# Kernel tuning notes

Hardware: AMD Instinct MI355X
Metric: run time of the kernel (lower is better)

## Reference

```python
import jax, jax.numpy as jnp
import numpy as np

L = 4          # GAT_LAYERS
HEADS = 4      # N_HEADS
H = 64         # transformer hidden dim
DH = H // HEADS
FIN = 32       # NODE_EMBED_SIZE
A = 15         # gats.num_actions (readout size)
OBS = 1500     # flattened obs dim
HS = 512       # hidden_size (policy FC)
NOUT = 15      # num_outputs
VH = 128       # VALUE_HIDDENS
B = 128        # batch of graphs
N = 1000       # nodes per map graph
TOT = B * N
DEG = 4
E = TOT * DEG


def _lin(key, fan_in, shape):
    return jax.random.normal(key, shape, jnp.float32) * (1.0 / np.sqrt(fan_in))


def setup_inputs() -> dict:
    key = jax.random.key(0)
    ks = jax.random.split(key, 30)
    node_feats = jax.random.normal(ks[0], (TOT, FIN), jnp.float32)
    obs = jax.random.normal(ks[1], (B, OBS), jnp.float32)
    # batched-graph edges: endpoints stay within each graph (DGL batch semantics)
    off = (jnp.arange(B) * N)[:, None]
    edge_src = (jax.random.randint(ks[2], (B, N * DEG), 0, N) + off).reshape(-1).astype(jnp.int32)
    edge_dst = (jax.random.randint(ks[3], (B, N * DEG), 0, N) + off).reshape(-1).astype(jnp.int32)
    agent_nodes = (jax.random.randint(ks[4], (B,), 0, N) + jnp.arange(B) * N).astype(jnp.int32)
    p = {
        'W_in': _lin(ks[5], FIN, (FIN, H)),
        'Wq': _lin(ks[6], H, (L, H, H)), 'Wk': _lin(ks[7], H, (L, H, H)),
        'Wv': _lin(ks[8], H, (L, H, H)), 'Wo': _lin(ks[9], H, (L, H, H)),
        'ln1_g': jnp.ones((L, H), jnp.float32), 'ln1_b': jnp.zeros((L, H), jnp.float32),
        'W1': _lin(ks[10], H, (L, H, 2 * H)), 'b1': jnp.zeros((L, 2 * H), jnp.float32),
        'W2': _lin(ks[11], 2 * H, (L, 2 * H, H)), 'b2': jnp.zeros((L, H), jnp.float32),
        'ln2_g': jnp.ones((L, H), jnp.float32), 'ln2_b': jnp.zeros((L, H), jnp.float32),
        'Wr': _lin(ks[12], H, (H, A)), 'br': jnp.zeros((A,), jnp.float32),
        'Wp1': _lin(ks[13], A + OBS, (A + OBS, HS)), 'bp1': jnp.zeros((HS,), jnp.float32),
        'Wp2': _lin(ks[14], HS, (HS, HS)), 'bp2': jnp.zeros((HS,), jnp.float32),
        'Wlog': _lin(ks[15], HS, (HS, NOUT)), 'blog': jnp.zeros((NOUT,), jnp.float32),
        'Wv1': _lin(ks[16], OBS, (OBS, VH)), 'bv1': jnp.zeros((VH,), jnp.float32),
        'Wv2': _lin(ks[17], VH, (VH, VH)), 'bv2': jnp.zeros((VH,), jnp.float32),
        'Wvo': _lin(ks[18], VH, (VH, 1)), 'bvo': jnp.zeros((1,), jnp.float32),
    }
    return dict(node_feats=node_feats, obs=obs, edge_src=edge_src, edge_dst=edge_dst,
                agent_nodes=agent_nodes, **p)


def _layernorm(x, g, b):
    m = x.mean(-1, keepdims=True)
    v = ((x - m) ** 2).mean(-1, keepdims=True)
    return (x - m) * jax.lax.rsqrt(v + 1e-5) * g + b


def reference(node_feats, obs, edge_src, edge_dst, agent_nodes, W_in, Wq, Wk, Wv, Wo,
              ln1_g, ln1_b, W1, b1, W2, b2, ln2_g, ln2_b, Wr, br,
              Wp1, bp1, Wp2, bp2, Wlog, blog, Wv1, bv1, Wv2, bv2, Wvo, bvo):
    n = node_feats.shape[0]
    x = node_feats @ W_in                                   # [n, H]
    inv_sqrt_dh = np.float32(1.0 / np.sqrt(DH))
    for l in range(L):
        q = (x @ Wq[l]).reshape(n, HEADS, DH)
        k = (x @ Wk[l]).reshape(n, HEADS, DH)
        v = (x @ Wv[l]).reshape(n, HEADS, DH)
        # per-edge attention scores, softmax over incoming edges of each dst node
        s = jnp.sum(q[edge_dst] * k[edge_src], axis=-1) * inv_sqrt_dh   # [E, HEADS]
        m = jax.ops.segment_max(s, edge_dst, num_segments=n)            # [n, HEADS]
        w = jnp.exp(s - m[edge_dst])
        denom = jax.ops.segment_sum(w, edge_dst, num_segments=n)        # [n, HEADS]
        agg = jax.ops.segment_sum(w[:, :, None] * v[edge_src], edge_dst, num_segments=n)
        attn = (agg / (denom[:, :, None] + 1e-9)).reshape(n, H) @ Wo[l]
        x = _layernorm(x + attn, ln1_g[l], ln1_b[l])
        h = jax.nn.relu(x @ W1[l] + b1[l]) @ W2[l] + b2[l]
        x = _layernorm(x + h, ln2_g[l], ln2_b[l])
    gat_out = x[agent_nodes] @ Wr + br                      # [B, A] per-agent action features
    feat = jnp.tanh(jnp.concatenate([gat_out, obs], axis=1) @ Wp1 + bp1)
    feat = jnp.tanh(feat @ Wp2 + bp2)
    logits = feat @ Wlog + blog                             # [B, NOUT]
    vh = jnp.tanh(obs @ Wv1 + bv1)
    vh = jnp.tanh(vh @ Wv2 + bv2)
    value = (vh @ Wvo + bvo)[:, 0]                          # [B]
    return logits, value
```

## Files before the change

### kernel.cpp

```cpp
#include <hip/hip_runtime.h>
#include <hip/hip_bf16.h>
#include <cstdint>
#include <cstddef>

#define DEV static __device__ __forceinline__

constexpr int GRAPHS = 128;
constexpr int NPG    = 1000;
constexpr int EPG    = 4000;
constexpr int TOTN   = GRAPHS * NPG;
constexpr int TOTE   = GRAPHS * EPG;
constexpr int HD     = 64;
constexpr int OBSD   = 1500;
constexpr int AD     = 15;

typedef __attribute__((ext_vector_type(8))) short bf16x8;
typedef __attribute__((ext_vector_type(4))) float f32x4;

DEV unsigned short f2b(float f){
  unsigned u = __float_as_uint(f);
  return (unsigned short)((u + 0x7fffu + ((u >> 16) & 1u)) >> 16);
}
DEV float b2f(unsigned short s){ return __uint_as_float((unsigned)s << 16); }

DEV void fma4(float4& a, float s, const float4 w){
  a.x = fmaf(s, w.x, a.x); a.y = fmaf(s, w.y, a.y);
  a.z = fmaf(s, w.z, a.z); a.w = fmaf(s, w.w, a.w);
}

DEV ushort4 pack4(float4 v){
  ushort4 r; r.x=f2b(v.x); r.y=f2b(v.y); r.z=f2b(v.z); r.w=f2b(v.w); return r;
}

__global__ __launch_bounds__(256) void k_wprep(const float* __restrict__ Wq,
    const float* __restrict__ Wk, const float* __restrict__ Wv,
    const float* __restrict__ Wo, const float* __restrict__ W1,
    const float* __restrict__ W2, unsigned short* __restrict__ wpack){
  int e = blockIdx.x*256 + threadIdx.x;
  int l = e >> 15;
  int r = e & 32767;
  float val;
  if (r < 12288){
    int c = r >> 6, k = r & 63;
    val = (c < 64)  ? Wq[l*4096 + k*64 + c]
        : (c < 128) ? Wk[l*4096 + k*64 + (c-64)]
                    : Wv[l*4096 + k*64 + (c-128)];
  } else if (r < 16384){
    int i = r - 12288; int c = i >> 6, k = i & 63;
    val = Wo[l*4096 + k*64 + c];
  } else if (r < 24576){
    int i = r - 16384; int c = i >> 6, k = i & 63;
    val = W1[l*8192 + k*128 + c];
  } else {
    int i = r - 24576; int c = i >> 7, k = i & 127;
    val = W2[l*8192 + k*64 + c];
  }
  wpack[e] = f2b(val);
}

__global__ __launch_bounds__(256) void k_zero(int* __restrict__ cnt){
  cnt[blockIdx.x*256 + threadIdx.x] = 0;
}

__global__ __launch_bounds__(256) void k_hist(const int* __restrict__ edst,
                                              int* __restrict__ cnt){
  int e = blockIdx.x*256 + threadIdx.x;
  atomicAdd(&cnt[edst[e]], 1);
}

__global__ __launch_bounds__(1024) void k_scan(const int* __restrict__ cnt,
    int* __restrict__ rstart, int* __restrict__ cursor){
  __shared__ int s[1024];
  const int g = blockIdx.x, tid = threadIdx.x;
  int v = (tid < NPG) ? cnt[g*NPG + tid] : 0;
  s[tid] = v;
  __syncthreads();
  #pragma unroll
  for (int off=1; off<1024; off<<=1){
    int t = (tid >= off) ? s[tid-off] : 0;
    __syncthreads();
    s[tid] += t;
    __syncthreads();
  }
  if (tid < NPG){
    int r = g*EPG + (s[tid] - v);
    rstart[g*NPG+tid] = r;
    cursor[g*NPG+tid] = r;
  }
}

__global__ __launch_bounds__(256) void k_scatter(const int* __restrict__ esrc,
    const int* __restrict__ edst, int* __restrict__ cursor,
    int* __restrict__ esorted){
  int e = blockIdx.x*256 + threadIdx.x;
  int pos = atomicAdd(&cursor[edst[e]], 1);
  esorted[pos] = esrc[e];
}

__global__ __launch_bounds__(256) void k_in(const float* __restrict__ nf,
                                            const float* __restrict__ Win,
                                            unsigned short* __restrict__ xb){
  __shared__ float  s_nf[256*36];
  __shared__ float4 s_w[512];
  const int tid = threadIdx.x;
  const int node0 = blockIdx.x * 256;
  const float4* W4 = (const float4*)Win;
  s_w[tid] = W4[tid]; s_w[tid+256] = W4[tid+256];
  const float4* nf4 = (const float4*)nf;
  float4* snf4 = (float4*)s_nf;
  #pragma unroll
  for (int r=0;r<8;r++){
    int i = tid + 256*r; int n = i>>3, k4 = i&7;
    snf4[n*9 + k4] = nf4[(size_t)(node0+n)*8 + k4];
  }
  __syncthreads();
  const int ng = tid>>2, cg = tid&3;
  float4 acc[4][4];
  #pragma unroll
  for (int i=0;i<4;i++){ acc[i][0]=make_float4(0,0,0,0); acc[i][1]=make_float4(0,0,0,0);
                         acc[i][2]=make_float4(0,0,0,0); acc[i][3]=make_float4(0,0,0,0); }
  #pragma unroll 4
  for (int k=0;k<32;k++){
    float nv[4];
    #pragma unroll
    for (int i=0;i<4;i++) nv[i] = s_nf[(ng + 64*i)*36 + k];
    float4 w[4];
    #pragma unroll
    for (int j=0;j<4;j++) w[j] = s_w[k*16 + cg*4 + j];
    #pragma unroll
    for (int i=0;i<4;i++){
      #pragma unroll
      for (int j=0;j<4;j++) fma4(acc[i][j], nv[i], w[j]);
    }
  }
  ushort4* xb4 = (ushort4*)xb;
  #pragma unroll
  for (int i=0;i<4;i++){
    size_t nidx = (size_t)(node0 + ng + 64*i) * 16;
    #pragma unroll
    for (int j=0;j<4;j++) xb4[nidx + cg*4 + j] = pack4(acc[i][j]);
  }
}

__global__ __launch_bounds__(256) void k_qkv_m(const unsigned short* __restrict__ xb,
    const unsigned short* __restrict__ wqkvT,
    unsigned short* __restrict__ qkv){
  __shared__ short s_w[192*72];
  __shared__ short s_st[4][16*200];
  const int tid = threadIdx.x;
  const int node0 = blockIdx.x * 256;
  {
    const unsigned* src = (const unsigned*)wqkvT;
    unsigned* dst = (unsigned*)s_w;
    #pragma unroll
    for (int r=0;r<24;r++){
      int j = tid + 256*r;
      int c = j >> 5, kk = j & 31;
      dst[c*36 + kk] = src[j];
    }
  }
  __syncthreads();
  const int lane = tid & 63, wave = tid >> 6;
  const int m = lane & 15, quad = lane >> 4;
  const int rowbase = node0 + wave*64;
  bf16x8 af[4][2];
  #pragma unroll
  for (int rt=0;rt<4;rt++){
    const unsigned short* xp = xb + (size_t)(rowbase + rt*16 + m)*64 + quad*8;
    af[rt][0] = *(const bf16x8*)xp;
    af[rt][1] = *(const bf16x8*)(xp + 32);
  }
  short* st = s_st[wave];
  #pragma unroll
  for (int rt=0;rt<4;rt++){
    #pragma unroll
    for (int ct=0;ct<12;ct++){
      bf16x8 b0 = *(const bf16x8*)&s_w[(ct*16+m)*72 + quad*8];
      bf16x8 b1 = *(const bf16x8*)&s_w[(ct*16+m)*72 + 32 + quad*8];
      f32x4 acc = {0.f,0.f,0.f,0.f};
      acc = __builtin_amdgcn_mfma_f32_16x16x32_bf16(af[rt][0], b0, acc, 0,0,0);
      acc = __builtin_amdgcn_mfma_f32_16x16x32_bf16(af[rt][1], b1, acc, 0,0,0);
      #pragma unroll
      for (int i=0;i<4;i++)
        st[(quad*4+i)*200 + ct*16 + m] = (short)f2b(acc[i]);
    }
    #pragma unroll
    for (int j=0;j<6;j++){
      int flat = (j*64 + lane)*8;
      int r = flat / 192, c = flat % 192;
      bf16x8 v = *(const bf16x8*)&st[r*200 + c];
      *(bf16x8*)(qkv + (size_t)(rowbase + rt*16 + r)*192 + c) = v;
    }
  }
}

__global__ __launch_bounds__(256) void k_edge2(const unsigned short* __restrict__ qkv,
    const int* __restrict__ rstart, const int* __restrict__ cnt,
    const int* __restrict__ esorted, unsigned short* __restrict__ attn_in){
  const int tid = threadIdx.x;
  const int wb = (blockIdx.x & 7)*1000 + (blockIdx.x >> 3);
  const int lane = tid & 63;
  const int sub  = lane >> 4;
  const int dg   = lane & 15;
  const int wave = tid >> 6;
  const int node = wb*16 + wave*4 + sub;
  const ushort4* row = (const ushort4*)(qkv + (size_t)node*192);
  ushort4 qu = row[dg];
  float q0 = b2f(qu.x), q1 = b2f(qu.y), q2 = b2f(qu.z), q3 = b2f(qu.w);
  const int rs = rstart[node];
  const int n  = cnt[node];
  float a0=0.f, a1=0.f, a2=0.f, a3=0.f, den=0.f;
  for (int i=0;i<n;i++){
    int src = esorted[rs + i];
    ushort4 ku = *(const ushort4*)(qkv + (size_t)src*192 + 64 + dg*4);
    ushort4 vu = *(const ushort4*)(qkv + (size_t)src*192 + 128 + dg*4);
    float p = q0*b2f(ku.x) + q1*b2f(ku.y) + q2*b2f(ku.z) + q3*b2f(ku.w);
    p += __shfl_xor(p, 1);
    p += __shfl_xor(p, 2);
    float w = __expf(p * 0.25f);
    den += w;
    a0 = fmaf(w, b2f(vu.x), a0);
    a1 = fmaf(w, b2f(vu.y), a1);
    a2 = fmaf(w, b2f(vu.z), a2);
    a3 = fmaf(w, b2f(vu.w), a3);
  }
  float inv = 1.0f/(den + 1e-9f);
  ushort4 o;
  o.x = f2b(a0*inv); o.y = f2b(a1*inv); o.z = f2b(a2*inv); o.w = f2b(a3*inv);
  ((ushort4*)attn_in)[(size_t)node*16 + dg] = o;
}

__global__ __launch_bounds__(256) void k_attn_m(const unsigned short* __restrict__ attn_in,
    const unsigned short* __restrict__ woT, const float* __restrict__ lg,
    const float* __restrict__ lb, unsigned short* __restrict__ xb){
  __shared__ short s_w[64*72];
  __shared__ short s_st[4][16*72];
  const int tid = threadIdx.x;
  const int node0 = blockIdx.x*256;
  {
    const unsigned* src = (const unsigned*)woT;
    unsigned* dst = (unsigned*)s_w;
    #pragma unroll
    for (int r=0;r<8;r++){
      int j = tid + 256*r;
      int c = j >> 5, kk = j & 31;
      dst[c*36 + kk] = src[j];
    }
  }
  __syncthreads();
  const int lane = tid&63, wave = tid>>6;
  const int m = lane&15, quad = lane>>4;
  const int rowbase = node0 + wave*64;
  bf16x8 bf[4][2];
  #pragma unroll
  for (int ct=0;ct<4;ct++){
    bf[ct][0] = *(const bf16x8*)&s_w[(ct*16+m)*72 + quad*8];
    bf[ct][1] = *(const bf16x8*)&s_w[(ct*16+m)*72 + 32 + quad*8];
  }
  float g[4], bb[4];
  #pragma unroll
  for (int ct=0;ct<4;ct++){ g[ct]=lg[ct*16+m]; bb[ct]=lb[ct*16+m]; }
  short* st = s_st[wave];
  #pragma unroll
  for (int rt=0;rt<4;rt++){
    const unsigned short* ap = attn_in + (size_t)(rowbase + rt*16 + m)*64 + quad*8;
    bf16x8 a0 = *(const bf16x8*)ap;
    bf16x8 a1 = *(const bf16x8*)(ap + 32);
    f32x4 acc[4];
    #pragma unroll
    for (int ct=0;ct<4;ct++){
      f32x4 z = {0.f,0.f,0.f,0.f};
      z = __builtin_amdgcn_mfma_f32_16x16x32_bf16(a0, bf[ct][0], z, 0,0,0);
      z = __builtin_amdgcn_mfma_f32_16x16x32_bf16(a1, bf[ct][1], z, 0,0,0);
      acc[ct] = z;
    }
    #pragma unroll
    for (int i=0;i<4;i++){
      size_t row = (size_t)(rowbase + rt*16 + quad*4 + i)*64;
      float v0 = acc[0][i] + b2f(xb[row + m]);
      float v1 = acc[1][i] + b2f(xb[row + 16 + m]);
      float v2 = acc[2][i] + b2f(xb[row + 32 + m]);
      float v3 = acc[3][i] + b2f(xb[row + 48 + m]);
      float sm = v0+v1+v2+v3;
      float sq = v0*v0+v1*v1+v2*v2+v3*v3;
      #pragma unroll
      for (int mk=1; mk<16; mk<<=1){ sm += __shfl_xor(sm, mk); sq += __shfl_xor(sq, mk); }
      float mean = sm*0.015625f;
      float var  = sq*0.015625f - mean*mean;
      float rs   = rsqrtf(var + 1e-5f);
      int rl = quad*4 + i;
      st[rl*72 + m]      = (short)f2b((v0-mean)*rs*g[0]+bb[0]);
      st[rl*72 + 16 + m] = (short)f2b((v1-mean)*rs*g[1]+bb[1]);
      st[rl*72 + 32 + m] = (short)f2b((v2-mean)*rs*g[2]+bb[2]);
      st[rl*72 + 48 + m] = (short)f2b((v3-mean)*rs*g[3]+bb[3]);
    }
    #pragma unroll
    for (int j=0;j<2;j++){
      int flat = (j*64 + lane)*8;
      int r = flat >> 6, c = flat & 63;
      bf16x8 v = *(const bf16x8*)&st[r*72 + c];
      *(bf16x8*)(xb + (size_t)(rowbase + rt*16 + r)*64 + c) = v;
    }
  }
}

__global__ __launch_bounds__(256) void k_ffn1_m(const unsigned short* __restrict__ xb,
    const unsigned short* __restrict__ w1T, const float* __restrict__ b1_l,
    unsigned short* __restrict__ h){
  __shared__ short s_w[128*72];
  __shared__ short s_st[4][16*136];
  const int tid = threadIdx.x;
  const int node0 = blockIdx.x*256;
  {
    const unsigned* src = (const unsigned*)w1T;
    unsigned* dst = (unsigned*)s_w;
    #pragma unroll
    for (int r=0;r<16;r++){
      int j = tid + 256*r;
      int c = j >> 5, kk = j & 31;
      dst[c*36 + kk] = src[j];
    }
  }
  __syncthreads();
  const int lane = tid&63, wave = tid>>6;
  const int m = lane&15, quad = lane>>4;
  const int rowbase = node0 + wave*64;
  bf16x8 af[4][2];
  #pragma unroll
  for (int rt=0;rt<4;rt++){
    const unsigned short* xp = xb + (size_t)(rowbase + rt*16 + m)*64 + quad*8;
    af[rt][0] = *(const bf16x8*)xp;
    af[rt][1] = *(const bf16x8*)(xp + 32);
  }
  short* st = s_st[wave];
  #pragma unroll
  for (int rt=0;rt<4;rt++){
    #pragma unroll
    for (int ct=0;ct<8;ct++){
      bf16x8 b0 = *(const bf16x8*)&s_w[(ct*16+m)*72 + quad*8];
      bf16x8 b1 = *(const bf16x8*)&s_w[(ct*16+m)*72 + 32 + quad*8];
      float bias = b1_l[ct*16+m];
      f32x4 acc = {0.f,0.f,0.f,0.f};
      acc = __builtin_amdgcn_mfma_f32_16x16x32_bf16(af[rt][0], b0, acc, 0,0,0);
      acc = __builtin_amdgcn_mfma_f32_16x16x32_bf16(af[rt][1], b1, acc, 0,0,0);
      #pragma unroll
      for (int i=0;i<4;i++)
        st[(quad*4+i)*136 + ct*16 + m] = (short)f2b(fmaxf(acc[i]+bias, 0.f));
    }
    #pragma unroll
    for (int j=0;j<4;j++){
      int flat = (j*64 + lane)*8;
      int r = flat >> 7, c = flat & 127;
      bf16x8 v = *(const bf16x8*)&st[r*136 + c];
      *(bf16x8*)(h + (size_t)(rowbase + rt*16 + r)*128 + c) = v;
    }
  }
}

__global__ __launch_bounds__(256) void k_ffn2_m(const unsigned short* __restrict__ h,
    const unsigned short* __restrict__ w2T, const float* __restrict__ b2_l,
    const float* __restrict__ lg, const float* __restrict__ lb,
    unsigned short* __restrict__ xb){
  __shared__ short s_w[64*136];
  __shared__ short s_st[4][16*72];
  const int tid = threadIdx.x;
  const int node0 = blockIdx.x*256;
  {
    const unsigned* src = (const unsigned*)w2T;
    unsigned* dst = (unsigned*)s_w;
    #pragma unroll
    for (int r=0;r<16;r++){
      int j = tid + 256*r;
      int c = j >> 6, kk = j & 63;
      dst[c*68 + kk] = src[j];
    }
  }
  __syncthreads();
  const int lane = tid&63, wave = tid>>6;
  const int m = lane&15, quad = lane>>4;
  const int rowbase = node0 + wave*64;
  bf16x8 bf[4][4];
  #pragma unroll
  for (int ct=0;ct<4;ct++){
    #pragma unroll
    for (int kc=0;kc<4;kc++)
      bf[ct][kc] = *(const bf16x8*)&s_w[(ct*16+m)*136 + kc*32 + quad*8];
  }
  float g[4], bb[4], b2v[4];
  #pragma unroll
  for (int ct=0;ct<4;ct++){ g[ct]=lg[ct*16+m]; bb[ct]=lb[ct*16+m]; b2v[ct]=b2_l[ct*16+m]; }
  short* st = s_st[wave];
  #pragma unroll
  for (int rt=0;rt<4;rt++){
    const unsigned short* ap = h + (size_t)(rowbase + rt*16 + m)*128 + quad*8;
    bf16x8 a0 = *(const bf16x8*)ap;
    bf16x8 a1 = *(const bf16x8*)(ap + 32);
    bf16x8 a2 = *(const bf16x8*)(ap + 64);
    bf16x8 a3 = *(const bf16x8*)(ap + 96);
    f32x4 acc[4];
    #pragma unroll
    for (int ct=0;ct<4;ct++){
      f32x4 z = {0.f,0.f,0.f,0.f};
      z = __builtin_amdgcn_mfma_f32_16x16x32_bf16(a0, bf[ct][0], z, 0,0,0);
      z = __builtin_amdgcn_mfma_f32_16x16x32_bf16(a1, bf[ct][1], z, 0,0,0);
      z = __builtin_amdgcn_mfma_f32_16x16x32_bf16(a2, bf[ct][2], z, 0,0,0);
      z = __builtin_amdgcn_mfma_f32_16x16x32_bf16(a3, bf[ct][3], z, 0,0,0);
      acc[ct] = z;
    }
    #pragma unroll
    for (int i=0;i<4;i++){
      size_t row = (size_t)(rowbase + rt*16 + quad*4 + i)*64;
      float v0 = acc[0][i] + b2v[0] + b2f(xb[row + m]);
      float v1 = acc[1][i] + b2v[1] + b2f(xb[row + 16 + m]);
      float v2 = acc[2][i] + b2v[2] + b2f(xb[row + 32 + m]);
      float v3 = acc[3][i] + b2v[3] + b2f(xb[row + 48 + m]);
      float sm = v0+v1+v2+v3;
      float sq = v0*v0+v1*v1+v2*v2+v3*v3;
      #pragma unroll
      for (int mk=1; mk<16; mk<<=1){ sm += __shfl_xor(sm, mk); sq += __shfl_xor(sq, mk); }
      float mean = sm*0.015625f;
      float var  = sq*0.015625f - mean*mean;
      float rs   = rsqrtf(var + 1e-5f);
      int rl = quad*4 + i;
      st[rl*72 + m]      = (short)f2b((v0-mean)*rs*g[0]+bb[0]);
      st[rl*72 + 16 + m] = (short)f2b((v1-mean)*rs*g[1]+bb[1]);
      st[rl*72 + 32 + m] = (short)f2b((v2-mean)*rs*g[2]+bb[2]);
      st[rl*72 + 48 + m] = (short)f2b((v3-mean)*rs*g[3]+bb[3]);
    }
    #pragma unroll
    for (int j=0;j<2;j++){
      int flat = (j*64 + lane)*8;
      int r = flat >> 6, c = flat & 63;
      bf16x8 v = *(const bf16x8*)&st[r*72 + c];
      *(bf16x8*)(xb + (size_t)(rowbase + rt*16 + r)*64 + c) = v;
    }
  }
}

__global__ __launch_bounds__(256) void k_feat(const unsigned short* __restrict__ xb,
    const float* __restrict__ obs, const int* __restrict__ agents,
    const float* __restrict__ Wr, const float* __restrict__ br,
    float* __restrict__ feat){
  __shared__ float s_xa[64];
  const int b = blockIdx.x, tid = threadIdx.x;
  if (tid < 64) s_xa[tid] = b2f(xb[(size_t)agents[b]*HD + tid]);
  __syncthreads();
  if (tid < AD){
    float a = br[tid];
    #pragma unroll 8
    for (int k=0;k<HD;k++) a = fmaf(s_xa[k], Wr[k*AD + tid], a);
    feat[(size_t)b*1536 + tid] = a;
  }
  for (int i=tid;i<OBSD;i+=256) feat[(size_t)b*1536 + AD + i] = obs[(size_t)b*OBSD + i];
  if (tid < 21) feat[(size_t)b*1536 + 1515 + tid] = 0.f;
}

template<int ROWS, int COLS, int CH, int KS, int N>
__global__ __launch_bounds__(ROWS*COLS) void k_gemm_part(
    const float* __restrict__ A, int lda, int K,
    const float* __restrict__ W, float* __restrict__ part){
  constexpr int BT = ROWS*COLS;
  __shared__ float s_a[ROWS*CH];
  const int tid = threadIdx.x;
  const int ct = blockIdx.x, rg = blockIdx.y, ks = blockIdx.z;
  const int chunk = (K + KS - 1) / KS;
  const int k0 = ks * chunk;
  const int len = min(K - k0, chunk);
  const int row0 = rg * ROWS;
  #pragma unroll
  for (int rr=0; rr<ROWS; rr++)
    for (int i=tid; i<len; i+=BT)
      s_a[rr*CH + i] = A[(size_t)(row0+rr)*lda + k0 + i];
  __syncthreads();
  const int r = tid / COLS, c = tid % COLS;
  const float* wp = W + (size_t)k0*N + ct*COLS + c;
  const float* ap = s_a + r*CH;
  float acc = 0.f;
  #pragma unroll 8
  for (int k=0;k<len;k++) acc = fmaf(ap[k], wp[(size_t)k*N], acc);
  part[((size_t)ks*128 + row0 + r)*N + ct*COLS + c] = acc;
}

template<int KS, int N, bool TANH>
__global__ __launch_bounds__(256) void k_reduce(const float* __restrict__ part,
    const float* __restrict__ bias, float* __restrict__ out, int MN){
  const int idx = blockIdx.x*256 + threadIdx.x;
  if (idx >= MN) return;
  float s = bias[idx & (N-1)];
  #pragma unroll
  for (int ks=0;ks<KS;ks++) s += part[(size_t)ks*MN + idx];
  out[idx] = TANH ? tanhf(s) : s;
}

__global__ __launch_bounds__(256) void k_logits(const float* __restrict__ f2,
    const float* __restrict__ Wlog, const float* __restrict__ blog,
    float* __restrict__ out){
  __shared__ float s_f[512];
  __shared__ float s_p[16*AD];
  const int b = blockIdx.x, tid = threadIdx.x;
  s_f[tid]     = f2[(size_t)b*512 + tid];
  s_f[tid+256] = f2[(size_t)b*512 + 256 + tid];
  __syncthreads();
  if (tid < 240){
    int c = tid % AD, kc = tid / AD;
    float a = 0.f;
    #pragma unroll 8
    for (int j=0;j<32;j++){ int k = kc*32 + j; a = fmaf(s_f[k], Wlog[k*AD + c], a); }
    s_p[tid] = a;
  }
  __syncthreads();
  if (tid < AD){
    float a = blog[tid];
    #pragma unroll
    for (int kc=0;kc<16;kc++) a += s_p[kc*AD + tid];
    out[(size_t)b*AD + tid] = a;
  }
}

__global__ __launch_bounds__(128) void k_vfin(const float* __restrict__ vh,
    const float* __restrict__ Wv2, const float* __restrict__ bv2,
    const float* __restrict__ Wvo, const float* __restrict__ bvo,
    float* __restrict__ out){
  __shared__ float s_v[128];
  __shared__ float s_r[128];
  const int b = blockIdx.x, tid = threadIdx.x;
  s_v[tid] = vh[(size_t)b*128 + tid];
  __syncthreads();
  float a = bv2[tid];
  #pragma unroll 8
  for (int k=0;k<128;k++) a = fmaf(s_v[k], Wv2[k*128 + tid], a);
  s_r[tid] = tanhf(a) * Wvo[tid];
  __syncthreads();
  if (tid < 64){
    float v = s_r[tid] + s_r[tid+64];
    #pragma unroll
    for (int m=32;m>=1;m>>=1) v += __shfl_xor(v, m);
    if (tid==0) out[GRAPHS*AD + b] = v + bvo[0];
  }
}

extern "C" void kernel_launch(void* const* d_in, const int* in_sizes, int n_in,
                              void* d_out, int out_size, void* d_ws, size_t ws_size,
                              hipStream_t stream) {
  (void)in_sizes; (void)n_in; (void)out_size; (void)ws_size;
  const float* nf     = (const float*)d_in[0];
  const float* obs    = (const float*)d_in[1];
  const int*   esrc   = (const int*)d_in[2];
  const int*   edst   = (const int*)d_in[3];
  const int*   agents = (const int*)d_in[4];
  const float* Win    = (const float*)d_in[5];
  const float* Wq     = (const float*)d_in[6];
  const float* Wk     = (const float*)d_in[7];
  const float* Wv     = (const float*)d_in[8];
  const float* Wo     = (const float*)d_in[9];
  const float* ln1g   = (const float*)d_in[10];
  const float* ln1b   = (const float*)d_in[11];
  const float* W1     = (const float*)d_in[12];
  const float* b1     = (const float*)d_in[13];
  const float* W2     = (const float*)d_in[14];
  const float* b2     = (const float*)d_in[15];
  const float* ln2g   = (const float*)d_in[16];
  const float* ln2b   = (const float*)d_in[17];
  const float* Wr     = (const float*)d_in[18];
  const float* br     = (const float*)d_in[19];
  const float* Wp1    = (const float*)d_in[20];
  const float* bp1    = (const float*)d_in[21];
  const float* Wp2    = (const float*)d_in[22];
  const float* bp2    = (const float*)d_in[23];
  const float* Wlog   = (const float*)d_in[24];
  const float* blog   = (const float*)d_in[25];
  const float* Wv1    = (const float*)d_in[26];
  const float* bv1    = (const float*)d_in[27];
  const float* Wv2    = (const float*)d_in[28];
  const float* bv2    = (const float*)d_in[29];
  const float* Wvo    = (const float*)d_in[30];
  const float* bvo    = (const float*)d_in[31];
  float* out = (float*)d_out;

  unsigned short* xb      = (unsigned short*)d_ws;
  unsigned short* qkv     = xb + (size_t)TOTN*HD;
  unsigned short* hbuf    = qkv;
  unsigned short* attn_in = qkv + (size_t)TOTN*192;
  unsigned short* wpack   = attn_in + (size_t)TOTN*HD;
  int* cnt     = (int*)(wpack + 131072);
  int* rstart  = cnt + TOTN;
  int* cursor  = rstart + TOTN;
  int* esorted = cursor + TOTN;
  float* feat = (float*)(esorted + TOTE);
  float* f1   = feat + 128*1536;
  float* f2   = f1 + 128*512;
  float* vh   = f2 + 128*512;
  float* part = vh + 128*128;

  k_wprep  <<<512, 256, 0, stream>>>(Wq, Wk, Wv, Wo, W1, W2, wpack);
  k_zero   <<<TOTN/256, 256, 0, stream>>>(cnt);
  k_hist   <<<TOTE/256, 256, 0, stream>>>(edst, cnt);
  k_scan   <<<GRAPHS, 1024, 0, stream>>>(cnt, rstart, cursor);
  k_scatter<<<TOTE/256, 256, 0, stream>>>(esrc, edst, cursor, esorted);

  k_in<<<TOTN/256, 256, 0, stream>>>(nf, Win, xb);
  for (int l=0; l<4; l++){
    const unsigned short* wl = wpack + l*32768;
    k_qkv_m <<<TOTN/256, 256, 0, stream>>>(xb, wl, qkv);
    k_edge2 <<<TOTN/16, 256, 0, stream>>>(qkv, rstart, cnt, esorted, attn_in);
    k_attn_m<<<TOTN/256, 256, 0, stream>>>(attn_in, wl + 12288,
                                           ln1g + l*64, ln1b + l*64, xb);
    k_ffn1_m<<<TOTN/256, 256, 0, stream>>>(xb, wl + 16384, b1 + l*128, hbuf);
    k_ffn2_m<<<TOTN/256, 256, 0, stream>>>(hbuf, wl + 24576, b2 + l*64,
                                           ln2g + l*64, ln2b + l*64, xb);
  }
  k_feat<<<GRAPHS, 256, 0, stream>>>(xb, obs, agents, Wr, br, feat);
  k_gemm_part<2,256,384,4,512><<<dim3(2,64,4), 512, 0, stream>>>(feat, 1536, 1515, Wp1, part);
  k_reduce<4,512,true><<<256, 256, 0, stream>>>(part, bp1, f1, 128*512);
  k_gemm_part<2,256,256,2,512><<<dim3(2,64,2), 512, 0, stream>>>(f1, 512, 512, Wp2, part);
  k_reduce<2,512,true><<<256, 256, 0, stream>>>(part, bp2, f2, 128*512);
  k_logits<<<GRAPHS, 256, 0, stream>>>(f2, Wlog, blog, out);
  k_gemm_part<4,128,192,8,128><<<dim3(1,32,8), 512, 0, stream>>>(obs, 1500, 1500, Wv1, part);
  k_reduce<8,128,true><<<64, 256, 0, stream>>>(part, bv1, vh, 128*128);
  k_vfin<<<GRAPHS, 128, 0, stream>>>(vh, Wv2, bv2, Wvo, bvo, out);
}
```

Before: 579.2 us.

## Fuse FFN1 and FFN2 into one kernel, shrink QKV staging buffer

Merges the two FFN kernels into one, so the 128-wide hidden activation stays in per-wave LDS staging and is fed straight into the second MFMA GEMM plus residual and layernorm. This removes a global write and read of the hidden buffer and one launch per layer. The QKV kernel now stages output in two halves of 96 columns, halving its staging LDS. The fused kernel holds both weight matrices in LDS (more shared memory per block), which may lower occupancy. It also reloads W2 fragments from LDS inside the loop instead of keeping them in registers.

```diff
diff --git a/kernel.cpp b/kernel.cpp
--- a/kernel.cpp
+++ b/kernel.cpp
@@ -146,7 +146,7 @@
     const unsigned short* __restrict__ wqkvT,
     unsigned short* __restrict__ qkv){
   __shared__ short s_w[192*72];
-  __shared__ short s_st[4][16*200];
+  __shared__ short s_st[4][16*104];
   const int tid = threadIdx.x;
   const int node0 = blockIdx.x * 256;
   {
@@ -174,22 +174,26 @@
   #pragma unroll
   for (int rt=0;rt<4;rt++){
     #pragma unroll
-    for (int ct=0;ct<12;ct++){
-      bf16x8 b0 = *(const bf16x8*)&s_w[(ct*16+m)*72 + quad*8];
-      bf16x8 b1 = *(const bf16x8*)&s_w[(ct*16+m)*72 + 32 + quad*8];
-      f32x4 acc = {0.f,0.f,0.f,0.f};
-      acc = __builtin_amdgcn_mfma_f32_16x16x32_bf16(af[rt][0], b0, acc, 0,0,0);
-      acc = __builtin_amdgcn_mfma_f32_16x16x32_bf16(af[rt][1], b1, acc, 0,0,0);
+    for (int half=0; half<2; half++){
       #pragma unroll
-      for (int i=0;i<4;i++)
-        st[(quad*4+i)*200 + ct*16 + m] = (short)f2b(acc[i]);
-    }
-    #pragma unroll
-    for (int j=0;j<6;j++){
-      int flat = (j*64 + lane)*8;
-      int r = flat / 192, c = flat % 192;
-      bf16x8 v = *(const bf16x8*)&st[r*200 + c];
-      *(bf16x8*)(qkv + (size_t)(rowbase + rt*16 + r)*192 + c) = v;
+      for (int c6=0;c6<6;c6++){
+        int ct = half*6 + c6;
+        bf16x8 b0 = *(const bf16x8*)&s_w[(ct*16+m)*72 + quad*8];
+        bf16x8 b1 = *(const bf16x8*)&s_w[(ct*16+m)*72 + 32 + quad*8];
+        f32x4 acc = {0.f,0.f,0.f,0.f};
+        acc = __builtin_amdgcn_mfma_f32_16x16x32_bf16(af[rt][0], b0, acc, 0,0,0);
+        acc = __builtin_amdgcn_mfma_f32_16x16x32_bf16(af[rt][1], b1, acc, 0,0,0);
+        #pragma unroll
+        for (int i=0;i<4;i++)
+          st[(quad*4+i)*104 + c6*16 + m] = (short)f2b(acc[i]);
+      }
+      #pragma unroll
+      for (int j=0;j<3;j++){
+        int flat = (j*64 + lane)*8;
+        int r = flat / 96, c = flat % 96;
+        bf16x8 v = *(const bf16x8*)&st[r*104 + c];
+        *(bf16x8*)(qkv + (size_t)(rowbase + rt*16 + r)*192 + half*96 + c) = v;
+      }
     }
   }
 }
@@ -304,16 +308,18 @@
   }
 }
 
-__global__ __launch_bounds__(256) void k_ffn1_m(const unsigned short* __restrict__ xb,
+__global__ __launch_bounds__(256) void k_ffn_m(unsigned short* __restrict__ xb,
     const unsigned short* __restrict__ w1T, const float* __restrict__ b1_l,
-    unsigned short* __restrict__ h){
-  __shared__ short s_w[128*72];
+    const unsigned short* __restrict__ w2T, const float* __restrict__ b2_l,
+    const float* __restrict__ lg, const float* __restrict__ lb){
+  __shared__ short s_w1[128*72];
+  __shared__ short s_w2[64*136];
   __shared__ short s_st[4][16*136];
   const int tid = threadIdx.x;
   const int node0 = blockIdx.x*256;
   {
     const unsigned* src = (const unsigned*)w1T;
-    unsigned* dst = (unsigned*)s_w;
+    unsigned* dst = (unsigned*)s_w1;
     #pragma unroll
     for (int r=0;r<16;r++){
       int j = tid + 256*r;
@@ -321,6 +327,16 @@
       dst[c*36 + kk] = src[j];
     }
   }
+  {
+    const unsigned* src = (const unsigned*)w2T;
+    unsigned* dst = (unsigned*)s_w2;
+    #pragma unroll
+    for (int r=0;r<16;r++){
+      int j = tid + 256*r;
+      int c = j >> 6, kk = j & 63;
+      dst[c*68 + kk] = src[j];
+    }
+  }
   __syncthreads();
   const int lane = tid&63, wave = tid>>6;
   const int m = lane&15, quad = lane>>4;
@@ -332,13 +348,16 @@
     af[rt][0] = *(const bf16x8*)xp;
     af[rt][1] = *(const bf16x8*)(xp + 32);
   }
+  float g[4], bb[4], b2v[4];
+  #pragma unroll
+  for (int ct=0;ct<4;ct++){ g[ct]=lg[ct*16+m]; bb[ct]=lb[ct*16+m]; b2v[ct]=b2_l[ct*16+m]; }
   short* st = s_st[wave];
   #pragma unroll
   for (int rt=0;rt<4;rt++){
     #pragma unroll
     for (int ct=0;ct<8;ct++){
-      bf16x8 b0 = *(const bf16x8*)&s_w[(ct*16+m)*72 + quad*8];
-      bf16x8 b1 = *(const bf16x8*)&s_w[(ct*16+m)*72 + 32 + quad*8];
+      bf16x8 b0 = *(const bf16x8*)&s_w1[(ct*16+m)*72 + quad*8];
+      bf16x8 b1 = *(const bf16x8*)&s_w1[(ct*16+m)*72 + 32 + quad*8];
       float bias = b1_l[ct*16+m];
       f32x4 acc = {0.f,0.f,0.f,0.f};
       acc = __builtin_amdgcn_mfma_f32_16x16x32_bf16(af[rt][0], b0, acc, 0,0,0);
@@ -347,73 +366,27 @@
       for (int i=0;i<4;i++)
         st[(quad*4+i)*136 + ct*16 + m] = (short)f2b(fmaxf(acc[i]+bias, 0.f));
     }
-    #pragma unroll
-    for (int j=0;j<4;j++){
-      int flat = (j*64 + lane)*8;
-      int r = flat >> 7, c = flat & 127;
-      bf16x8 v = *(const bf16x8*)&st[r*136 + c];
-      *(bf16x8*)(h + (size_t)(rowbase + rt*16 + r)*128 + c) = v;
-    }
-  }
-}
-
-__global__ __launch_bounds__(256) void k_ffn2_m(const unsigned short* __restrict__ h,
-    const unsigned short* __restrict__ w2T, const float* __restrict__ b2_l,
-    const float* __restrict__ lg, const float* __restrict__ lb,
-    unsigned short* __restrict__ xb){
-  __shared__ short s_w[64*136];
-  __shared__ short s_st[4][16*72];
-  const int tid = threadIdx.x;
-  const int node0 = blockIdx.x*256;
-  {
-    const unsigned* src = (const unsigned*)w2T;
-    unsigned* dst = (unsigned*)s_w;
-    #pragma unroll
-    for (int r=0;r<16;r++){
-      int j = tid + 256*r;
-      int c = j >> 6, kk = j & 63;
-      dst[c*68 + kk] = src[j];
-    }
-  }
-  __syncthreads();
-  const int lane = tid&63, wave = tid>>6;
-  const int m = lane&15, quad = lane>>4;
-  const int rowbase = node0 + wave*64;
-  bf16x8 bf[4][4];
-  #pragma unroll
-  for (int ct=0;ct<4;ct++){
-    #pragma unroll
-    for (int kc=0;kc<4;kc++)
-      bf[ct][kc] = *(const bf16x8*)&s_w[(ct*16+m)*136 + kc*32 + quad*8];
-  }
-  float g[4], bb[4], b2v[4];
-  #pragma unroll
-  for (int ct=0;ct<4;ct++){ g[ct]=lg[ct*16+m]; bb[ct]=lb[ct*16+m]; b2v[ct]=b2_l[ct*16+m]; }
-  short* st = s_st[wave];
-  #pragma unroll
-  for (int rt=0;rt<4;rt++){
-    const unsigned short* ap = h + (size_t)(rowbase + rt*16 + m)*128 + quad*8;
-    bf16x8 a0 = *(const bf16x8*)ap;
-    bf16x8 a1 = *(const bf16x8*)(ap + 32);
-    bf16x8 a2 = *(const bf16x8*)(ap + 64);
-    bf16x8 a3 = *(const bf16x8*)(ap + 96);
-    f32x4 acc[4];
+    bf16x8 h0 = *(const bf16x8*)&st[m*136 + quad*8];
+    bf16x8 h1 = *(const bf16x8*)&st[m*136 + 32 + quad*8];
+    bf16x8 h2 = *(const bf16x8*)&st[m*136 + 64 + quad*8];
+    bf16x8 h3 = *(const bf16x8*)&st[m*136 + 96 + quad*8];
+    f32x4 acc2[4];
     #pragma unroll
     for (int ct=0;ct<4;ct++){
       f32x4 z = {0.f,0.f,0.f,0.f};
-      z = __builtin_amdgcn_mfma_f32_16x16x32_bf16(a0, bf[ct][0], z, 0,0,0);
-      z = __builtin_amdgcn_mfma_f32_16x16x32_bf16(a1, bf[ct][1], z, 0,0,0);
-      z = __builtin_amdgcn_mfma_f32_16x16x32_bf16(a2, bf[ct][2], z, 0,0,0);
-      z = __builtin_amdgcn_mfma_f32_16x16x32_bf16(a3, bf[ct][3], z, 0,0,0);
-      acc[ct] = z;
+      z = __builtin_amdgcn_mfma_f32_16x16x32_bf16(h0, *(const bf16x8*)&s_w2[(ct*16+m)*136 + quad*8],      z, 0,0,0);
+      z = __builtin_amdgcn_mfma_f32_16x16x32_bf16(h1, *(const bf16x8*)&s_w2[(ct*16+m)*136 + 32 + quad*8], z, 0,0,0);
+      z = __builtin_amdgcn_mfma_f32_16x16x32_bf16(h2, *(const bf16x8*)&s_w2[(ct*16+m)*136 + 64 + quad*8], z, 0,0,0);
+      z = __builtin_amdgcn_mfma_f32_16x16x32_bf16(h3, *(const bf16x8*)&s_w2[(ct*16+m)*136 + 96 + quad*8], z, 0,0,0);
+      acc2[ct] = z;
     }
     #pragma unroll
     for (int i=0;i<4;i++){
       size_t row = (size_t)(rowbase + rt*16 + quad*4 + i)*64;
-      float v0 = acc[0][i] + b2v[0] + b2f(xb[row + m]);
-      float v1 = acc[1][i] + b2v[1] + b2f(xb[row + 16 + m]);
-      float v2 = acc[2][i] + b2v[2] + b2f(xb[row + 32 + m]);
-      float v3 = acc[3][i] + b2v[3] + b2f(xb[row + 48 + m]);
+      float v0 = acc2[0][i] + b2v[0] + b2f(xb[row + m]);
+      float v1 = acc2[1][i] + b2v[1] + b2f(xb[row + 16 + m]);
+      float v2 = acc2[2][i] + b2v[2] + b2f(xb[row + 32 + m]);
+      float v3 = acc2[3][i] + b2v[3] + b2f(xb[row + 48 + m]);
       float sm = v0+v1+v2+v3;
       float sq = v0*v0+v1*v1+v2*v2+v3*v3;
       #pragma unroll
@@ -422,16 +395,16 @@
       float var  = sq*0.015625f - mean*mean;
       float rs   = rsqrtf(var + 1e-5f);
       int rl = quad*4 + i;
-      st[rl*72 + m]      = (short)f2b((v0-mean)*rs*g[0]+bb[0]);
-      st[rl*72 + 16 + m] = (short)f2b((v1-mean)*rs*g[1]+bb[1]);
-      st[rl*72 + 32 + m] = (short)f2b((v2-mean)*rs*g[2]+bb[2]);
-      st[rl*72 + 48 + m] = (short)f2b((v3-mean)*rs*g[3]+bb[3]);
+      st[rl*136 + m]      = (short)f2b((v0-mean)*rs*g[0]+bb[0]);
+      st[rl*136 + 16 + m] = (short)f2b((v1-mean)*rs*g[1]+bb[1]);
+      st[rl*136 + 32 + m] = (short)f2b((v2-mean)*rs*g[2]+bb[2]);
+      st[rl*136 + 48 + m] = (short)f2b((v3-mean)*rs*g[3]+bb[3]);
     }
     #pragma unroll
     for (int j=0;j<2;j++){
       int flat = (j*64 + lane)*8;
       int r = flat >> 6, c = flat & 63;
-      bf16x8 v = *(const bf16x8*)&st[r*72 + c];
+      bf16x8 v = *(const bf16x8*)&st[r*136 + c];
       *(bf16x8*)(xb + (size_t)(rowbase + rt*16 + r)*64 + c) = v;
     }
   }
@@ -579,7 +552,6 @@
 
   unsigned short* xb      = (unsigned short*)d_ws;
   unsigned short* qkv     = xb + (size_t)TOTN*HD;
-  unsigned short* hbuf    = qkv;
   unsigned short* attn_in = qkv + (size_t)TOTN*192;
   unsigned short* wpack   = attn_in + (size_t)TOTN*HD;
   int* cnt     = (int*)(wpack + 131072);
@@ -605,9 +577,9 @@
     k_edge2 <<<TOTN/16, 256, 0, stream>>>(qkv, rstart, cnt, esorted, attn_in);
     k_attn_m<<<TOTN/256, 256, 0, stream>>>(attn_in, wl + 12288,
                                            ln1g + l*64, ln1b + l*64, xb);
-    k_ffn1_m<<<TOTN/256, 256, 0, stream>>>(xb, wl + 16384, b1 + l*128, hbuf);
-    k_ffn2_m<<<TOTN/256, 256, 0, stream>>>(hbuf, wl + 24576, b2 + l*64,
-                                           ln2g + l*64, ln2b + l*64, xb);
+    k_ffn_m <<<TOTN/256, 256, 0, stream>>>(xb, wl + 16384, b1 + l*128,
+                                           wl + 24576, b2 + l*64,
+                                           ln2g + l*64, ln2b + l*64);
   }
   k_feat<<<GRAPHS, 256, 0, stream>>>(xb, obs, agents, Wr, br, feat);
   k_gemm_part<2,256,384,4,512><<<dim3(2,64,4), 512, 0, stream>>>(feat, 1536, 1515, Wp1, part);
```

Result: faster. 534.5 us (-7.7%).
